# Kernel optimization log

Measured on AMD Instinct MI355X. Metric: run time of the kernel, lower is better.

Reference implementation:

```python
import jax, jax.numpy as jnp
import numpy as np

B, T, ENC, TAG, HG, HE, M = 64, 383, 768, 128, 400, 256, 20
D = ENC + TAG          # graph RNN input size (encoder_output_dim + tag_representation_dim)
S = T + 1              # +1 for head sentinel


def setup_inputs() -> dict:
    ks = jax.random.split(jax.random.key(0), 16)
    g = lambda i, shape, s=0.05: jax.random.normal(ks[i], shape, dtype=jnp.float32) * s
    z = lambda n: jnp.zeros((n,), jnp.float32)
    return dict(
        input=g(0, (B, T, ENC), 1.0),
        tag_embeddings=g(1, (B, T, TAG), 1.0),
        mask=jnp.ones((B, T), jnp.int32),
        head_sentinel=g(2, (D,), 1.0),
        # bidirectional graph RNN (tanh, 1 layer)
        Wih_f=g(3, (HG, D)), Whh_f=g(4, (HG, HG)), bih_f=z(HG), bhh_f=z(HG),
        Wih_b=g(5, (HG, D)), Whh_b=g(6, (HG, HG)), bih_b=z(HG), bhh_b=z(HG),
        # graph_to_edge projection (edge RNN initial hidden)
        Wg2e=g(7, (HE, 2 * HG)), bg2e=z(HE),
        # edge RNN (past direction, input size 1) + edge classifier head
        Wih_e=g(8, (HE, 1)), Whh_e=g(9, (HE, HE)), bih_e=z(HE), bhh_e=z(HE),
        Wcls=g(10, (1, HE)), bcls=z(1),
        bos=z(1),
        # head/dep tag feedforwards
        Wht=g(11, (TAG, 2 * HG)), bht=z(TAG),
        Wdt=g(12, (TAG, 2 * HG)), bdt=z(TAG),
    )


def _masked_rnn(x, m, Wih, Whh, bih, bhh, reverse):
    # x: [B,S,D], m: [B,S,1]. Emulates packed nn.RNN(tanh) for one direction:
    # hidden only advances on valid steps (so the backward direction starts its
    # recurrence at each sequence's true length), outputs are zero on padding
    # (matching pad_packed_sequence zero padding).
    def step(h, inp):
        xt, mt = inp
        hn = jnp.tanh(xt @ Wih.T + bih + h @ Whh.T + bhh)
        h = mt * hn + (1.0 - mt) * h
        return h, h * mt

    h0 = jnp.zeros((x.shape[0], Wih.shape[0]), x.dtype)
    _, ys = jax.lax.scan(step, h0, (x.swapaxes(0, 1), m.swapaxes(0, 1)), reverse=reverse)
    return ys.swapaxes(0, 1)


def reference(input, tag_embeddings, mask, head_sentinel,
              Wih_f, Whh_f, bih_f, bhh_f, Wih_b, Whh_b, bih_b, bhh_b,
              Wg2e, bg2e, Wih_e, Whh_e, bih_e, bhh_e, Wcls, bcls, bos,
              Wht, bht, Wdt, bdt):
    x = jnp.concatenate([input, tag_embeddings], axis=-1)            # [B,T,D]
    sent = jnp.broadcast_to(head_sentinel, (B, 1, D))
    x = jnp.concatenate([sent, x], axis=1)                           # [B,S,D]
    m = jnp.concatenate([jnp.ones((B, 1), mask.dtype), mask], axis=1)  # sentinel is valid
    mf = m.astype(x.dtype)[..., None]                                # [B,S,1]

    fwd = _masked_rnn(x, mf, Wih_f, Whh_f, bih_f, bhh_f, reverse=False)
    bwd = _masked_rnn(x, mf, Wih_b, Whh_b, bih_b, bhh_b, reverse=True)
    graph_state = jnp.concatenate([fwd, bwd], axis=-1)               # [B,S,2*HG]

    # initial hidden = graph_to_edge(graph_state), input starts at bos, then
    # feeds back the previous logit.
    proj = graph_state.reshape(B * S, 2 * HG) @ Wg2e.T + bg2e        # [B*S,HE]
    steps = min(M, S)
    x0 = jnp.broadcast_to(bos.reshape(1, 1), (B * S, 1))

    def estep(carry, _):
        xe, h = carry
        hn = jnp.tanh(xe @ Wih_e.T + bih_e + h @ Whh_e.T + bhh_e)
        logit = hn @ Wcls.T + bcls                                   # [B*S,1]
        return (logit, hn), logit

    _, logits = jax.lax.scan(estep, (x0, proj), None, length=steps)  # [steps,B*S,1]
    Ap = logits.squeeze(-1).T.reshape(B, S, steps)                   # [B,S,steps]

    # banded scatter: arc_logits[:, i, start:i] = Ap[:, i, :i-start], start=max(0,i-M)
    rows = jnp.arange(S)[:, None]
    cols = jnp.arange(S)[None, :]
    start = jnp.maximum(0, rows - M)
    k = cols - start
    valid = (cols >= start) & (cols < rows)
    idx = jnp.clip(k, 0, steps - 1)
    band = Ap[:, jnp.broadcast_to(rows, (S, S)), jnp.broadcast_to(idx, (S, S))]  # [B,S,S]
    arc_logits = jnp.where(valid[None], band, jnp.zeros((), Ap.dtype))

    # tag feedforwards (Dropout is identity in eval)
    head_tag = jax.nn.elu(graph_state @ Wht.T + bht)
    dep_tag = jax.nn.elu(graph_state @ Wdt.T + bdt)
    return head_tag, dep_tag, arc_logits
```

## Files before the change

### kernel.cpp

```cpp
#include <hip/hip_runtime.h>

#define B_ 64
#define T_ 383
#define S_ 384
#define ENC_ 768
#define TAGD_ 128
#define D_ 896
#define HG_ 400
#define HE_ 256
#define MSTEP_ 20
#define RTOT_ (B_*S_)
#define HEAD_SZ_ ((size_t)RTOT_*TAGD_)

typedef short short8 __attribute__((ext_vector_type(8)));
typedef float f32x4 __attribute__((ext_vector_type(4)));

__device__ __forceinline__ float bf2f(unsigned short u){
  union { unsigned int i; float f; } v; v.i = ((unsigned int)u) << 16; return v.f;
}
__device__ __forceinline__ unsigned short f2bf(float f){
  union { float f; unsigned int i; } v; v.f = f;
  unsigned int r = (v.i + 0x7fffu + ((v.i >> 16) & 1u)) >> 16;
  return (unsigned short)r;
}
__device__ __forceinline__ float tanh_fast(float x){
  float xc = fminf(fmaxf(x, -15.f), 15.f);
  float e = __expf(2.f*xc);
  return (e - 1.f) * __builtin_amdgcn_rcpf(e + 1.f);
}

__device__ __forceinline__ void probe_maps(int lane, int* mlab, int* nlab){
  unsigned short lb = f2bf((float)(lane & 15));
  short8 av, bv;
  #pragma unroll
  for (int j = 0; j < 8; j++){ av[j] = (short)lb; bv[j] = (short)0x3F80; }
  f32x4 z = {0.f,0.f,0.f,0.f};
  f32x4 d1 = __builtin_amdgcn_mfma_f32_16x16x32_bf16(av, bv, z, 0, 0, 0);
  f32x4 d2 = __builtin_amdgcn_mfma_f32_16x16x32_bf16(bv, av, z, 0, 0, 0);
  #pragma unroll
  for (int i = 0; i < 4; i++){
    mlab[i] = (int)(d1[i]*0.03125f + 0.5f);
    nlab[i] = (int)(d2[i]*0.03125f + 0.5f);
  }
}

__global__ __launch_bounds__(256) void cvt4(const float* __restrict__ src,
                                            unsigned short* __restrict__ dst, int n4)
{
  int i = blockIdx.x*256 + threadIdx.x;
  if (i >= n4) return;
  float4 v = ((const float4*)src)[i];
  ((ushort4*)dst)[i] = make_ushort4(f2bf(v.x), f2bf(v.y), f2bf(v.z), f2bf(v.w));
}

__global__ __launch_bounds__(256) void pack_wrnn3(const float* __restrict__ Wf,
                                                  const float* __restrict__ Wb,
                                                  unsigned short* __restrict__ Wr)
{
  int idx = blockIdx.x*256 + threadIdx.x;
  if (idx >= 2*26*13*16*32) return;
  int dir = idx / (26*13*16*32);
  int rem = idx % (26*13*16*32);
  int tile = rem / (13*16*32); rem %= (13*16*32);
  int kt = rem / (16*32);      rem %= (16*32);
  int r  = rem / 32;
  int kk = rem % 32;
  int n = tile*16 + r, k = kt*32 + kk;
  unsigned short v = 0;
  if (n < HG_ && k < HG_) v = f2bf((dir ? Wb : Wf)[(size_t)n*HG_ + k]);
  Wr[idx] = v;
}

__global__ __launch_bounds__(64) void maskpack(const int* __restrict__ mask,
                                               unsigned long long* __restrict__ mb)
{
  int t = blockIdx.x; int b = threadIdx.x;
  int m = (t > 0) ? mask[b*T_ + (t-1)] : 1;
  unsigned long long v = __ballot(m != 0);
  if (b == 0) mb[t] = v;
}

__global__ __launch_bounds__(256) void gemm_pre(
    const float* __restrict__ inp, const float* __restrict__ tag,
    const float* __restrict__ sent, const unsigned short* __restrict__ W,
    const float* __restrict__ bihf, const float* __restrict__ bhhf,
    const float* __restrict__ bihb, const float* __restrict__ bhhb,
    unsigned short* __restrict__ preT2)
{
  int wid = blockIdx.x*4 + (threadIdx.x >> 6);
  int lane = threadIdx.x & 63;
  int q = lane >> 4, l16 = lane & 15;
  int mt = wid / 25, ct = wid % 25;
  int r = mt*16 + l16;
  int s = r % S_, b = r / S_;
  int mlab[4], nlab[4];
  probe_maps(lane, mlab, nlab);
  int n0 = ct*32 + l16, n1 = n0 + 16;
  const unsigned short* w0 = W + (size_t)n0*D_;
  const unsigned short* w1 = W + (size_t)n1*D_;
  f32x4 acc0 = {0.f,0.f,0.f,0.f}, acc1 = {0.f,0.f,0.f,0.f};
  for (int k0 = 0; k0 < D_; k0 += 32){
    int k = k0 + q*8;
    const float* asrc = (s == 0) ? (sent + k)
        : ((k < ENC_) ? inp + (size_t)(b*T_ + (s-1))*ENC_ + k
                      : tag + (size_t)(b*T_ + (s-1))*TAGD_ + (k - ENC_));
    float4 v0 = *(const float4*)asrc;
    float4 v1 = *(const float4*)(asrc + 4);
    short8 a;
    a[0]=(short)f2bf(v0.x); a[1]=(short)f2bf(v0.y); a[2]=(short)f2bf(v0.z); a[3]=(short)f2bf(v0.w);
    a[4]=(short)f2bf(v1.x); a[5]=(short)f2bf(v1.y); a[6]=(short)f2bf(v1.z); a[7]=(short)f2bf(v1.w);
    acc0 = __builtin_amdgcn_mfma_f32_16x16x32_bf16(a, *(const short8*)(w0 + k), acc0, 0,0,0);
    acc1 = __builtin_amdgcn_mfma_f32_16x16x32_bf16(a, *(const short8*)(w1 + k), acc1, 0,0,0);
  }
  #pragma unroll
  for (int i = 0; i < 4; i++){
    int row = mt*16 + mlab[i];
    int c0 = ct*32 + nlab[i], c1 = c0 + 16;
    int bb = row / S_, ss = row % S_;
    int mtb = bb >> 4, qb = (bb >> 2) & 3, rib = bb & 3;
    float v0 = acc0[i] + ((c0 < HG_) ? (bihf[c0] + bhhf[c0]) : (bihb[c0-HG_] + bhhb[c0-HG_]));
    float v1 = acc1[i] + ((c1 < HG_) ? (bihf[c1] + bhhf[c1]) : (bihb[c1-HG_] + bhhb[c1-HG_]));
    {
      int d = (c0 >= HG_) ? 1 : 0; int nn = c0 - d*HG_;
      int nt = nn >> 4, lc = nn & 15;
      preT2[((((size_t)(d*S_ + ss)*25 + nt)*4 + mtb)*64 + (qb*16 + lc))*4 + rib] = f2bf(v0);
    }
    {
      int d = (c1 >= HG_) ? 1 : 0; int nn = c1 - d*HG_;
      int nt = nn >> 4, lc = nn & 15;
      preT2[((((size_t)(d*S_ + ss)*25 + nt)*4 + mtb)*64 + (qb*16 + lc))*4 + rib] = f2bf(v1);
    }
  }
}

#define HSTR5_ 424
template<int NTC>
__device__ void rnn_body5(int nt0, int dir, int bg, int lane, int tid,
    const unsigned short* __restrict__ pD,
    const unsigned short* __restrict__ Wd,
    const unsigned long long* __restrict__ mbits,
    unsigned short* __restrict__ gs,
    unsigned short (*Hh)[HSTR5_], unsigned short (*Hl)[HSTR5_])
{
  int q = lane >> 4, l16 = lane & 15;
  const unsigned short* wrow[NTC];
  #pragma unroll
  for (int j = 0; j < NTC; j++)
    wrow[j] = Wd + (size_t)(nt0 + j)*13*512 + l16*32 + q*8;

  short8 bh[NTC][6];
  #pragma unroll
  for (int j = 0; j < NTC; j++)
    #pragma unroll
    for (int kt = 0; kt < 6; kt++)
      bh[j][kt] = *(const short8*)(wrow[j] + kt*512);

  for (int stp = 0; stp < S_; stp++){
    int t = dir ? (S_ - 1 - stp) : stp;
    unsigned long long mb = mbits[t];
    bool allm = (mb == 0xFFFFFFFFFFFFFFFFull);
    const unsigned short* pT = pD + (size_t)t*25600;

    ushort4 pu[NTC];
    #pragma unroll
    for (int j = 0; j < NTC; j++)
      pu[j] = *(const ushort4*)(pT + (((size_t)(nt0 + j)*4 + bg)*64 + lane)*4);

    f32x4 acc[NTC];
    #pragma unroll
    for (int j = 0; j < NTC; j++) acc[j] = (f32x4){0.f,0.f,0.f,0.f};

    #pragma unroll
    for (int kt = 6; kt < 13; kt++){
      short8 bv[NTC];
      #pragma unroll
      for (int j = 0; j < NTC; j++) bv[j] = *(const short8*)(wrow[j] + kt*512);
      short8 ah = *(const short8*)&Hh[l16][kt*32 + q*8];
      short8 al = *(const short8*)&Hl[l16][kt*32 + q*8];
      #pragma unroll
      for (int j = 0; j < NTC; j++){
        acc[j] = __builtin_amdgcn_mfma_f32_16x16x32_bf16(ah, bv[j], acc[j], 0,0,0);
        acc[j] = __builtin_amdgcn_mfma_f32_16x16x32_bf16(al, bv[j], acc[j], 0,0,0);
      }
    }
    #pragma unroll
    for (int kt = 0; kt < 6; kt++){
      short8 ah = *(const short8*)&Hh[l16][kt*32 + q*8];
      short8 al = *(const short8*)&Hl[l16][kt*32 + q*8];
      #pragma unroll
      for (int j = 0; j < NTC; j++){
        acc[j] = __builtin_amdgcn_mfma_f32_16x16x32_bf16(ah, bh[j][kt], acc[j], 0,0,0);
        acc[j] = __builtin_amdgcn_mfma_f32_16x16x32_bf16(al, bh[j][kt], acc[j], 0,0,0);
      }
    }

    __syncthreads();

    #pragma unroll
    for (int j = 0; j < NTC; j++){
      int n = (nt0 + j)*16 + l16;
      unsigned short pv[4] = {pu[j].x, pu[j].y, pu[j].z, pu[j].w};
      #pragma unroll
      for (int ri = 0; ri < 4; ri++){
        int b = q*4 + ri;
        float hn = tanh_fast(acc[j][ri] + bf2f(pv[ri]));
        float hnew;
        if (allm) hnew = hn;
        else {
          bool mv = (mb >> (bg*16 + b)) & 1ull;
          float hold = bf2f(Hh[b][n]) + bf2f(Hl[b][n]);
          hnew = mv ? hn : hold;
        }
        unsigned short hi = f2bf(hnew);
        Hh[b][n] = hi;
        Hl[b][n] = f2bf(hnew - bf2f(hi));
      }
    }
    __syncthreads();

    for (int c = tid; c < 800; c += 512){
      int b = c / 50, off = c - b*50;
      uint4 dv = *(const uint4*)&Hh[b][off*8];
      bool mv = (mb >> (bg*16 + b)) & 1ull;
      uint4 z = make_uint4(0,0,0,0);
      *(uint4*)(gs + (size_t)((bg*16 + b)*S_ + t)*800 + dir*HG_ + off*8) = mv ? dv : z;
    }
  }
}

__global__ __launch_bounds__(512, 1) void rnn_mfma5(
    const unsigned short* __restrict__ preT2, const unsigned short* __restrict__ Wr,
    const unsigned long long* __restrict__ mbits, unsigned short* __restrict__ gs)
{
  __shared__ __align__(16) unsigned short Hh[16][HSTR5_];
  __shared__ __align__(16) unsigned short Hl[16][HSTR5_];
  int tid = threadIdx.x;
  int wave = tid >> 6, lane = tid & 63;
  int dir = blockIdx.x >> 2, bg = blockIdx.x & 3;
  for (int i = tid; i < 16*HSTR5_/2; i += 512){
    ((unsigned int*)Hh)[i] = 0u;
    ((unsigned int*)Hl)[i] = 0u;
  }
  __syncthreads();
  const unsigned short* Wd = Wr + (size_t)dir*26*13*512;
  const unsigned short* pD = preT2 + (size_t)dir*S_*25600;
  if (wave == 0) rnn_body5<4>(0,                dir, bg, lane, tid, pD, Wd, mbits, gs, Hh, Hl);
  else           rnn_body5<3>(4 + (wave-1)*3,   dir, bg, lane, tid, pD, Wd, mbits, gs, Hh, Hl);
}

__global__ __launch_bounds__(256) void gemm_proj(
    const unsigned short* __restrict__ gs, const unsigned short* __restrict__ Wg2e,
    const float* __restrict__ bg2e, float* __restrict__ proj)
{
  int wid = blockIdx.x*4 + (threadIdx.x >> 6);
  int lane = threadIdx.x & 63;
  int q = lane >> 4, l16 = lane & 15;
  int mt = wid >> 3, ct = wid & 7;
  int mlab[4], nlab[4];
  probe_maps(lane, mlab, nlab);
  const unsigned short* arow = gs + (size_t)(mt*16 + l16)*800;
  int n0 = ct*32 + l16, n1 = n0 + 16;
  const unsigned short* w0 = Wg2e + (size_t)n0*800;
  const unsigned short* w1 = Wg2e + (size_t)n1*800;
  f32x4 acc0 = {0.f,0.f,0.f,0.f}, acc1 = {0.f,0.f,0.f,0.f};
  for (int k0 = 0; k0 < 800; k0 += 32){
    int k = k0 + q*8;
    short8 a = *(const short8*)(arow + k);
    acc0 = __builtin_amdgcn_mfma_f32_16x16x32_bf16(a, *(const short8*)(w0 + k), acc0, 0,0,0);
    acc1 = __builtin_amdgcn_mfma_f32_16x16x32_bf16(a, *(const short8*)(w1 + k), acc1, 0,0,0);
  }
  #pragma unroll
  for (int i = 0; i < 4; i++){
    int row = mt*16 + mlab[i];
    int c0 = ct*32 + nlab[i], c1 = c0 + 16;
    proj[(size_t)row*HE_ + c0] = acc0[i] + bg2e[c0];
    proj[(size_t)row*HE_ + c1] = acc1[i] + bg2e[c1];
  }
}

__global__ __launch_bounds__(256) void gemm_tag(
    const unsigned short* __restrict__ gs, const unsigned short* __restrict__ Wtag,
    const float* __restrict__ bht, const float* __restrict__ bdt,
    float* __restrict__ outH)
{
  int wid = blockIdx.x*4 + (threadIdx.x >> 6);
  int lane = threadIdx.x & 63;
  int q = lane >> 4, l16 = lane & 15;
  int mt = wid >> 3, ct = wid & 7;
  int mlab[4], nlab[4];
  probe_maps(lane, mlab, nlab);
  const unsigned short* arow = gs + (size_t)(mt*16 + l16)*800;
  int n0 = ct*32 + l16, n1 = n0 + 16;
  const unsigned short* w0 = Wtag + (size_t)n0*800;
  const unsigned short* w1 = Wtag + (size_t)n1*800;
  f32x4 acc0 = {0.f,0.f,0.f,0.f}, acc1 = {0.f,0.f,0.f,0.f};
  for (int k0 = 0; k0 < 800; k0 += 32){
    int k = k0 + q*8;
    short8 a = *(const short8*)(arow + k);
    acc0 = __builtin_amdgcn_mfma_f32_16x16x32_bf16(a, *(const short8*)(w0 + k), acc0, 0,0,0);
    acc1 = __builtin_amdgcn_mfma_f32_16x16x32_bf16(a, *(const short8*)(w1 + k), acc1, 0,0,0);
  }
  #pragma unroll
  for (int i = 0; i < 4; i++){
    int row = mt*16 + mlab[i];
    int c0 = ct*32 + nlab[i], c1 = c0 + 16;
    float v0 = acc0[i] + ((c0 < TAGD_) ? bht[c0] : bdt[c0-TAGD_]);
    float v1 = acc1[i] + ((c1 < TAGD_) ? bht[c1] : bdt[c1-TAGD_]);
    v0 = (v0 > 0.f) ? v0 : expm1f(v0);
    v1 = (v1 > 0.f) ? v1 : expm1f(v1);
    if (c0 < TAGD_) outH[(size_t)row*TAGD_ + c0] = v0;
    else            outH[HEAD_SZ_ + (size_t)row*TAGD_ + (c0-TAGD_)] = v0;
    if (c1 < TAGD_) outH[(size_t)row*TAGD_ + c1] = v1;
    else            outH[HEAD_SZ_ + (size_t)row*TAGD_ + (c1-TAGD_)] = v1;
  }
}

#define EROWS_ 96
#define ESTR_ 264
__global__ __launch_bounds__(256, 1) void estep2(
    const float* __restrict__ proj, const unsigned short* __restrict__ WhhE,
    const float* __restrict__ bihE, const float* __restrict__ bhhE,
    const float* __restrict__ WihE, const float* __restrict__ Wcls,
    const float* __restrict__ bclsp, const float* __restrict__ bosp,
    float* __restrict__ Ap)
{
  __shared__ __align__(16) unsigned short H[2][EROWS_][ESTR_];
  __shared__ float lacc[4][EROWS_];
  __shared__ float xls[EROWS_];
  int tid = threadIdx.x;
  int wave = tid >> 6, lane = tid & 63, q = lane >> 4, l16 = lane & 15;
  size_t rowbase = (size_t)blockIdx.x * EROWS_;

  short8 bw[4][8];
  float bias_n[4], wcl_n[4], wih_n[4];
  #pragma unroll
  for (int nt = 0; nt < 4; nt++){
    int n = wave*64 + nt*16 + l16;
    #pragma unroll
    for (int kt = 0; kt < 8; kt++)
      bw[nt][kt] = *(const short8*)(WhhE + (size_t)n*HE_ + kt*32 + q*8);
    bias_n[nt] = bihE[n] + bhhE[n];
    wcl_n[nt]  = Wcls[n];
    wih_n[nt]  = WihE[n];
  }
  for (int i = tid; i < EROWS_*HE_; i += 256){
    int r = i >> 8, n = i & 255;
    H[0][r][n] = f2bf(proj[(rowbase + r)*HE_ + n]);
  }
  if (tid < EROWS_) xls[tid] = bosp[0];
  float bc = bclsp[0];
  __syncthreads();

  for (int stp = 0; stp < MSTEP_; stp++){
    int cur = stp & 1, nxt = cur ^ 1;
    float lp[6][4];
    #pragma unroll
    for (int mt = 0; mt < 6; mt++){
      short8 af[8];
      #pragma unroll
      for (int kt = 0; kt < 8; kt++)
        af[kt] = *(const short8*)&H[cur][mt*16 + l16][kt*32 + q*8];
      float xr[4];
      #pragma unroll
      for (int ri = 0; ri < 4; ri++) xr[ri] = xls[mt*16 + q*4 + ri];
      f32x4 acc[4];
      #pragma unroll
      for (int nt = 0; nt < 4; nt++) acc[nt] = (f32x4){0.f,0.f,0.f,0.f};
      #pragma unroll
      for (int kt = 0; kt < 8; kt++){
        #pragma unroll
        for (int nt = 0; nt < 4; nt++)
          acc[nt] = __builtin_amdgcn_mfma_f32_16x16x32_bf16(af[kt], bw[nt][kt], acc[nt], 0,0,0);
      }
      #pragma unroll
      for (int ri = 0; ri < 4; ri++) lp[mt][ri] = 0.f;
      #pragma unroll
      for (int nt = 0; nt < 4; nt++){
        int n = wave*64 + nt*16 + l16;
        #pragma unroll
        for (int ri = 0; ri < 4; ri++){
          float v = acc[nt][ri] + bias_n[nt] + xr[ri]*wih_n[nt];
          float h = tanh_fast(v);
          lp[mt][ri] += h * wcl_n[nt];
          H[nxt][mt*16 + q*4 + ri][n] = f2bf(h);
        }
      }
    }
    #pragma unroll
    for (int mt = 0; mt < 6; mt++){
      #pragma unroll
      for (int ri = 0; ri < 4; ri++){
        float v = lp[mt][ri];
        v += __shfl_xor(v, 1, 16);
        v += __shfl_xor(v, 2, 16);
        v += __shfl_xor(v, 4, 16);
        v += __shfl_xor(v, 8, 16);
        lp[mt][ri] = v;
      }
    }
    if (l16 == 0){
      #pragma unroll
      for (int mt = 0; mt < 6; mt++)
        #pragma unroll
        for (int ri = 0; ri < 4; ri++)
          lacc[wave][mt*16 + q*4 + ri] = lp[mt][ri];
    }
    __syncthreads();
    if (tid < EROWS_){
      float lg = lacc[0][tid] + lacc[1][tid] + lacc[2][tid] + lacc[3][tid] + bc;
      Ap[(rowbase + tid)*MSTEP_ + stp] = lg;
      xls[tid] = lg;
    }
    __syncthreads();
  }
}

__global__ __launch_bounds__(256) void band_kernel(const float* __restrict__ Ap,
                                                   float* __restrict__ arc)
{
  int idx = blockIdx.x*256 + threadIdx.x;
  int c = idx % S_;
  int rr = (idx / S_) % S_;
  int b = idx / (S_*S_);
  int start = rr - MSTEP_; if (start < 0) start = 0;
  bool valid = (c >= start) && (c < rr);
  float v = 0.f;
  if (valid) v = Ap[(size_t)(b*S_ + rr)*MSTEP_ + (c - start)];
  arc[idx] = v;
}

extern "C" void kernel_launch(void* const* d_in, const int* in_sizes, int n_in,
                              void* d_out, int out_size, void* d_ws, size_t ws_size,
                              hipStream_t stream)
{
  const float* inp  = (const float*)d_in[0];
  const float* tag  = (const float*)d_in[1];
  const int*   mask = (const int*)d_in[2];
  const float* sent = (const float*)d_in[3];
  const float* Wihf = (const float*)d_in[4];
  const float* Whhf = (const float*)d_in[5];
  const float* bihf = (const float*)d_in[6];
  const float* bhhf = (const float*)d_in[7];
  const float* Wihb = (const float*)d_in[8];
  const float* Whhb = (const float*)d_in[9];
  const float* bihb = (const float*)d_in[10];
  const float* bhhb = (const float*)d_in[11];
  const float* Wg2e = (const float*)d_in[12];
  const float* bg2e = (const float*)d_in[13];
  const float* WihE = (const float*)d_in[14];
  const float* WhhE = (const float*)d_in[15];
  const float* bihE = (const float*)d_in[16];
  const float* bhhE = (const float*)d_in[17];
  const float* Wcls = (const float*)d_in[18];
  const float* bcls = (const float*)d_in[19];
  const float* bos  = (const float*)d_in[20];
  const float* Wht  = (const float*)d_in[21];
  const float* bht  = (const float*)d_in[22];
  const float* Wdt  = (const float*)d_in[23];
  const float* bdt  = (const float*)d_in[24];
  (void)in_sizes; (void)n_in; (void)out_size; (void)ws_size;

  char* ws = (char*)d_ws;
  unsigned short* preT2  = (unsigned short*)ws;
  unsigned short* gs     = (unsigned short*)(ws + 39321600);
  unsigned short* Wrnn3  = (unsigned short*)(ws + 78643200);
  unsigned short* Wihcat = (unsigned short*)(ws + 79335424);
  unsigned short* Wg2e_b = (unsigned short*)(ws + 80769024);
  unsigned short* Wtag_b = (unsigned short*)(ws + 81178624);
  unsigned short* WhhE_b = (unsigned short*)(ws + 81588224);
  unsigned long long* maskb = (unsigned long long*)(ws + 81719296);
  float*          proj   = (float*)ws;
  float*          Ap     = (float*)(ws + 25165824);

  float* outH   = (float*)d_out;
  float* outArc = outH + 2*HEAD_SZ_;

  hipLaunchKernelGGL(cvt4, dim3(350), dim3(256), 0, stream, Wihf, Wihcat,           400*896/4);
  hipLaunchKernelGGL(cvt4, dim3(350), dim3(256), 0, stream, Wihb, Wihcat + 400*896, 400*896/4);
  hipLaunchKernelGGL(cvt4, dim3(200), dim3(256), 0, stream, Wg2e, Wg2e_b,           256*800/4);
  hipLaunchKernelGGL(cvt4, dim3(100), dim3(256), 0, stream, Wht,  Wtag_b,           128*800/4);
  hipLaunchKernelGGL(cvt4, dim3(100), dim3(256), 0, stream, Wdt,  Wtag_b + 128*800, 128*800/4);
  hipLaunchKernelGGL(cvt4, dim3(64),  dim3(256), 0, stream, WhhE, WhhE_b,           256*256/4);
  hipLaunchKernelGGL(pack_wrnn3, dim3(1352), dim3(256), 0, stream, Whhf, Whhb, Wrnn3);
  hipLaunchKernelGGL(maskpack, dim3(S_), dim3(64), 0, stream, mask, maskb);
  hipLaunchKernelGGL(gemm_pre, dim3(9600), dim3(256), 0, stream,
                     inp, tag, sent, Wihcat, bihf, bhhf, bihb, bhhb, preT2);
  hipLaunchKernelGGL(rnn_mfma5, dim3(8), dim3(512), 0, stream, preT2, Wrnn3, maskb, gs);
  hipLaunchKernelGGL(gemm_proj, dim3(3072), dim3(256), 0, stream, gs, Wg2e_b, bg2e, proj);
  hipLaunchKernelGGL(gemm_tag,  dim3(3072), dim3(256), 0, stream, gs, Wtag_b, bht, bdt, outH);
  hipLaunchKernelGGL(estep2, dim3(256), dim3(256), 0, stream,
                     proj, WhhE_b, bihE, bhhE, WihE, Wcls, bcls, bos, Ap);
  hipLaunchKernelGGL(band_kernel, dim3(36864), dim3(256), 0, stream, Ap, outArc);
}
```

Before: 2.284 ms.

## Keep full recurrent weights in registers and use packed bf16 convert

The serial graph RNN kernel is rebalanced. Each of the 8 waves now holds all 13 k-tiles of its 3 column tiles of Whh in registers, instead of reloading 7 of the 13 tiles from global memory on every one of the 384 timesteps. Wave 0 takes the 25th column tile as an extra, still streamed from memory. This cuts per-step global weight traffic on the latency-critical recurrence but raises register pressure to about 156 VGPRs of weights per lane. Separately, the input-projection GEMM replaces the software fp32-to-bf16 rounding with the packed v_cvt_pk_bf16_f32 instruction.

```diff
diff --git a/kernel.cpp b/kernel.cpp
--- a/kernel.cpp
+++ b/kernel.cpp
@@ -106,9 +106,12 @@
                       : tag + (size_t)(b*T_ + (s-1))*TAGD_ + (k - ENC_));
     float4 v0 = *(const float4*)asrc;
     float4 v1 = *(const float4*)(asrc + 4);
-    short8 a;
-    a[0]=(short)f2bf(v0.x); a[1]=(short)f2bf(v0.y); a[2]=(short)f2bf(v0.z); a[3]=(short)f2bf(v0.w);
-    a[4]=(short)f2bf(v1.x); a[5]=(short)f2bf(v1.y); a[6]=(short)f2bf(v1.z); a[7]=(short)f2bf(v1.w);
+    union { unsigned int u[4]; short8 s8; } au;
+    asm("v_cvt_pk_bf16_f32 %0, %1, %2" : "=v"(au.u[0]) : "v"(v0.x), "v"(v0.y));
+    asm("v_cvt_pk_bf16_f32 %0, %1, %2" : "=v"(au.u[1]) : "v"(v0.z), "v"(v0.w));
+    asm("v_cvt_pk_bf16_f32 %0, %1, %2" : "=v"(au.u[2]) : "v"(v1.x), "v"(v1.y));
+    asm("v_cvt_pk_bf16_f32 %0, %1, %2" : "=v"(au.u[3]) : "v"(v1.z), "v"(v1.w));
+    short8 a = au.s8;
     acc0 = __builtin_amdgcn_mfma_f32_16x16x32_bf16(a, *(const short8*)(w0 + k), acc0, 0,0,0);
     acc1 = __builtin_amdgcn_mfma_f32_16x16x32_bf16(a, *(const short8*)(w1 + k), acc1, 0,0,0);
   }
@@ -134,8 +137,30 @@
 }
 
 #define HSTR5_ 424
-template<int NTC>
-__device__ void rnn_body5(int nt0, int dir, int bg, int lane, int tid,
+__device__ __forceinline__ void rnn_epi6(int n, const f32x4& acc, const ushort4& pu,
+    unsigned long long mb, bool allm, int bg, int q,
+    unsigned short (*Hh)[HSTR5_], unsigned short (*Hl)[HSTR5_])
+{
+  unsigned short pv[4] = {pu.x, pu.y, pu.z, pu.w};
+  #pragma unroll
+  for (int ri = 0; ri < 4; ri++){
+    int b = q*4 + ri;
+    float hn = tanh_fast(acc[ri] + bf2f(pv[ri]));
+    float hnew;
+    if (allm) hnew = hn;
+    else {
+      bool mv = (mb >> (bg*16 + b)) & 1ull;
+      float hold = bf2f(Hh[b][n]) + bf2f(Hl[b][n]);
+      hnew = mv ? hn : hold;
+    }
+    unsigned short hi = f2bf(hnew);
+    Hh[b][n] = hi;
+    Hl[b][n] = f2bf(hnew - bf2f(hi));
+  }
+}
+
+template<bool EXTRA>
+__device__ void rnn_body6(int nt0, int dir, int bg, int lane, int tid,
     const unsigned short* __restrict__ pD,
     const unsigned short* __restrict__ Wd,
     const unsigned long long* __restrict__ mbits,
@@ -143,17 +168,16 @@
     unsigned short (*Hh)[HSTR5_], unsigned short (*Hl)[HSTR5_])
 {
   int q = lane >> 4, l16 = lane & 15;
-  const unsigned short* wrow[NTC];
-  #pragma unroll
-  for (int j = 0; j < NTC; j++)
-    wrow[j] = Wd + (size_t)(nt0 + j)*13*512 + l16*32 + q*8;
-
-  short8 bh[NTC][6];
-  #pragma unroll
-  for (int j = 0; j < NTC; j++)
-    #pragma unroll
-    for (int kt = 0; kt < 6; kt++)
-      bh[j][kt] = *(const short8*)(wrow[j] + kt*512);
+
+  short8 bh[3][13];
+  #pragma unroll
+  for (int j = 0; j < 3; j++){
+    const unsigned short* wr = Wd + (size_t)(nt0 + j)*13*512 + l16*32 + q*8;
+    #pragma unroll
+    for (int kt = 0; kt < 13; kt++)
+      bh[j][kt] = *(const short8*)(wr + kt*512);
+  }
+  const unsigned short* wx = Wd + (size_t)24*13*512 + l16*32 + q*8;
 
   for (int stp = 0; stp < S_; stp++){
     int t = dir ? (S_ - 1 - stp) : stp;
@@ -161,34 +185,28 @@
     bool allm = (mb == 0xFFFFFFFFFFFFFFFFull);
     const unsigned short* pT = pD + (size_t)t*25600;
 
-    ushort4 pu[NTC];
-    #pragma unroll
-    for (int j = 0; j < NTC; j++)
+    ushort4 pu[3]; ushort4 pux = make_ushort4(0,0,0,0);
+    #pragma unroll
+    for (int j = 0; j < 3; j++)
       pu[j] = *(const ushort4*)(pT + (((size_t)(nt0 + j)*4 + bg)*64 + lane)*4);
-
-    f32x4 acc[NTC];
-    #pragma unroll
-    for (int j = 0; j < NTC; j++) acc[j] = (f32x4){0.f,0.f,0.f,0.f};
-
-    #pragma unroll
-    for (int kt = 6; kt < 13; kt++){
-      short8 bv[NTC];
-      #pragma unroll
-      for (int j = 0; j < NTC; j++) bv[j] = *(const short8*)(wrow[j] + kt*512);
+    if (EXTRA)
+      pux = *(const ushort4*)(pT + (((size_t)24*4 + bg)*64 + lane)*4);
+
+    f32x4 acc[3]; f32x4 accx = {0.f,0.f,0.f,0.f};
+    #pragma unroll
+    for (int j = 0; j < 3; j++) acc[j] = (f32x4){0.f,0.f,0.f,0.f};
+
+    #pragma unroll
+    for (int kt = 0; kt < 13; kt++){
       short8 ah = *(const short8*)&Hh[l16][kt*32 + q*8];
       short8 al = *(const short8*)&Hl[l16][kt*32 + q*8];
-      #pragma unroll
-      for (int j = 0; j < NTC; j++){
-        acc[j] = __builtin_amdgcn_mfma_f32_16x16x32_bf16(ah, bv[j], acc[j], 0,0,0);
-        acc[j] = __builtin_amdgcn_mfma_f32_16x16x32_bf16(al, bv[j], acc[j], 0,0,0);
+      if (EXTRA){
+        short8 bx = *(const short8*)(wx + kt*512);
+        accx = __builtin_amdgcn_mfma_f32_16x16x32_bf16(ah, bx, accx, 0,0,0);
+        accx = __builtin_amdgcn_mfma_f32_16x16x32_bf16(al, bx, accx, 0,0,0);
       }
-    }
-    #pragma unroll
-    for (int kt = 0; kt < 6; kt++){
-      short8 ah = *(const short8*)&Hh[l16][kt*32 + q*8];
-      short8 al = *(const short8*)&Hl[l16][kt*32 + q*8];
-      #pragma unroll
-      for (int j = 0; j < NTC; j++){
+      #pragma unroll
+      for (int j = 0; j < 3; j++){
         acc[j] = __builtin_amdgcn_mfma_f32_16x16x32_bf16(ah, bh[j][kt], acc[j], 0,0,0);
         acc[j] = __builtin_amdgcn_mfma_f32_16x16x32_bf16(al, bh[j][kt], acc[j], 0,0,0);
       }
@@ -197,25 +215,11 @@
     __syncthreads();
 
     #pragma unroll
-    for (int j = 0; j < NTC; j++){
-      int n = (nt0 + j)*16 + l16;
-      unsigned short pv[4] = {pu[j].x, pu[j].y, pu[j].z, pu[j].w};
-      #pragma unroll
-      for (int ri = 0; ri < 4; ri++){
-        int b = q*4 + ri;
-        float hn = tanh_fast(acc[j][ri] + bf2f(pv[ri]));
-        float hnew;
-        if (allm) hnew = hn;
-        else {
-          bool mv = (mb >> (bg*16 + b)) & 1ull;
-          float hold = bf2f(Hh[b][n]) + bf2f(Hl[b][n]);
-          hnew = mv ? hn : hold;
-        }
-        unsigned short hi = f2bf(hnew);
-        Hh[b][n] = hi;
-        Hl[b][n] = f2bf(hnew - bf2f(hi));
-      }
-    }
+    for (int j = 0; j < 3; j++)
+      rnn_epi6((nt0 + j)*16 + l16, acc[j], pu[j], mb, allm, bg, q, Hh, Hl);
+    if (EXTRA)
+      rnn_epi6(24*16 + l16, accx, pux, mb, allm, bg, q, Hh, Hl);
+
     __syncthreads();
 
     for (int c = tid; c < 800; c += 512){
@@ -228,7 +232,7 @@
   }
 }
 
-__global__ __launch_bounds__(512, 1) void rnn_mfma5(
+__global__ __launch_bounds__(512, 1) void rnn_mfma6(
     const unsigned short* __restrict__ preT2, const unsigned short* __restrict__ Wr,
     const unsigned long long* __restrict__ mbits, unsigned short* __restrict__ gs)
 {
@@ -244,8 +248,8 @@
   __syncthreads();
   const unsigned short* Wd = Wr + (size_t)dir*26*13*512;
   const unsigned short* pD = preT2 + (size_t)dir*S_*25600;
-  if (wave == 0) rnn_body5<4>(0,                dir, bg, lane, tid, pD, Wd, mbits, gs, Hh, Hl);
-  else           rnn_body5<3>(4 + (wave-1)*3,   dir, bg, lane, tid, pD, Wd, mbits, gs, Hh, Hl);
+  if (wave == 0) rnn_body6<true >(0,       dir, bg, lane, tid, pD, Wd, mbits, gs, Hh, Hl);
+  else           rnn_body6<false>(wave*3,  dir, bg, lane, tid, pD, Wd, mbits, gs, Hh, Hl);
 }
 
 __global__ __launch_bounds__(256) void gemm_proj(
@@ -485,7 +489,7 @@
   hipLaunchKernelGGL(maskpack, dim3(S_), dim3(64), 0, stream, mask, maskb);
   hipLaunchKernelGGL(gemm_pre, dim3(9600), dim3(256), 0, stream,
                      inp, tag, sent, Wihcat, bihf, bhhf, bihb, bhhb, preT2);
-  hipLaunchKernelGGL(rnn_mfma5, dim3(8), dim3(512), 0, stream, preT2, Wrnn3, maskb, gs);
+  hipLaunchKernelGGL(rnn_mfma6, dim3(8), dim3(512), 0, stream, preT2, Wrnn3, maskb, gs);
   hipLaunchKernelGGL(gemm_proj, dim3(3072), dim3(256), 0, stream, gs, Wg2e_b, bg2e, proj);
   hipLaunchKernelGGL(gemm_tag,  dim3(3072), dim3(256), 0, stream, gs, Wtag_b, bht, bdt, outH);
   hipLaunchKernelGGL(estep2, dim3(256), dim3(256), 0, stream,
```

Result: no change. 2.313 ms (+1.3%).
